# Optimization experiments

Hardware: AMD Instinct MI355X
Metric: run time of the kernel (lower is better)

The kernel has to match this reference:

```python
import jax, jax.numpy as jnp
import numpy as np

TOP_K = 2


def setup_inputs() -> dict:
    key = jax.random.key(0)
    ks = jax.random.split(key, 5)
    B, S, H, E, F = 2, 4096, 2048, 8, 4096
    scale_h = 1.0 / np.sqrt(H)
    scale_f = 1.0 / np.sqrt(F)
    return {
        "hidden_states": jax.random.normal(ks[0], (B, S, H), jnp.float32),
        "gate_w": jax.random.normal(ks[1], (E, H), jnp.float32) * scale_h,
        "w1": jax.random.normal(ks[2], (E, F, H), jnp.float32) * scale_h,
        "w3": jax.random.normal(ks[3], (E, F, H), jnp.float32) * scale_h,
        "w2": jax.random.normal(ks[4], (E, H, F), jnp.float32) * scale_f,
    }


def reference(hidden_states, gate_w, w1, w3, w2):
    B, S, H = hidden_states.shape
    E = gate_w.shape[0]
    x = hidden_states.reshape(-1, H)                      # [T, H]
    T = x.shape[0]

    # Router: logits -> softmax(fp32) -> top-k -> renormalize
    router_logits = x @ gate_w.T                          # [T, E]
    probs = jax.nn.softmax(router_logits.astype(jnp.float32), axis=-1)
    topk_w, topk_idx = jax.lax.top_k(probs, TOP_K)        # [T, k]
    topk_w = topk_w / jnp.sum(topk_w, axis=-1, keepdims=True)
    topk_w = topk_w.astype(x.dtype)

    # Per-expert combine weight (0 for unselected experts) [T, E]
    combine = jnp.sum(jax.nn.one_hot(topk_idx, E, dtype=x.dtype)
                      * topk_w[..., None], axis=1)

    # Expert SwiGLU MLPs, weighted-accumulated (loop over fixed E=8)
    out = jnp.zeros((T, H), dtype=x.dtype)
    for e in range(E):
        h = jax.nn.silu(x @ w1[e].T) * (x @ w3[e].T)      # [T, F]
        out = out + (h @ w2[e].T) * combine[:, e:e + 1]   # [T, H]

    return out.reshape(B, S, H), router_logits
```

## Files before the change

### kernel.cpp

```cpp
#include <hip/hip_runtime.h>
#include <math.h>

#define T_TOK 8192
#define H_DIM 2048
#define F_DIM 4096
#define E_NUM 8
#define MAXPAIR (T_TOK * 2)
#define MAX_MT 136
#define BM 128
#define BN 128
#define BK 32

typedef __attribute__((ext_vector_type(4))) float f32x4;
typedef __attribute__((ext_vector_type(8))) short s16x8;
typedef __attribute__((ext_vector_type(8))) __bf16 bf16x8;
typedef __attribute__((ext_vector_type(4))) unsigned short u16x4;

__device__ __forceinline__ unsigned short f2bf(float f) {
  unsigned int u = __float_as_uint(f);
  u += 0x7FFFu + ((u >> 16) & 1u);
  return (unsigned short)(u >> 16);
}

__device__ __forceinline__ s16x8 pack8(f32x4 a, f32x4 b) {
  s16x8 r;
  r[0] = (short)f2bf(a.x); r[1] = (short)f2bf(a.y);
  r[2] = (short)f2bf(a.z); r[3] = (short)f2bf(a.w);
  r[4] = (short)f2bf(b.x); r[5] = (short)f2bf(b.y);
  r[6] = (short)f2bf(b.z); r[7] = (short)f2bf(b.w);
  return r;
}

#define GLD16(gsrc, ldst)                                                      \
  __builtin_amdgcn_global_load_lds(                                            \
      (__attribute__((address_space(1))) void*)(gsrc),                         \
      (__attribute__((address_space(3))) void*)(ldst), 16, 0, 0)

__global__ __launch_bounds__(256) void convert_kernel(
    const float* __restrict__ src, unsigned short* __restrict__ dst,
    long long n8) {
  long long i = (long long)blockIdx.x * 256 + threadIdx.x;
  const long long stride = (long long)gridDim.x * 256;
  for (; i < n8; i += stride) {
    f32x4 a = *(const f32x4*)(src + i * 8);
    f32x4 b = *(const f32x4*)(src + i * 8 + 4);
    *(s16x8*)(dst + i * 8) = pack8(a, b);
  }
}

__global__ __launch_bounds__(256) void router_kernel(
    const float* __restrict__ x, const float* __restrict__ gw,
    float* __restrict__ logits, unsigned short* __restrict__ xb,
    int* __restrict__ ctrl, int* __restrict__ tIdx, float* __restrict__ tW) {
  const int wid = threadIdx.x >> 6, lane = threadIdx.x & 63;
  const int t = blockIdx.x * 4 + wid;
  const float* xr = x + (size_t)t * H_DIM;
  float acc[E_NUM];
#pragma unroll
  for (int e = 0; e < E_NUM; ++e) acc[e] = 0.f;
#pragma unroll
  for (int c = 0; c < H_DIM / 256; ++c) {
    const int h0 = c * 256 + lane * 4;
    f32x4 xv = *(const f32x4*)(xr + h0);
    u16x4 p;
    p.x = f2bf(xv.x); p.y = f2bf(xv.y); p.z = f2bf(xv.z); p.w = f2bf(xv.w);
    *(u16x4*)(xb + (size_t)t * H_DIM + h0) = p;
#pragma unroll
    for (int e = 0; e < E_NUM; ++e) {
      f32x4 gv = *(const f32x4*)(gw + (size_t)e * H_DIM + h0);
      acc[e] += xv.x * gv.x + xv.y * gv.y + xv.z * gv.z + xv.w * gv.w;
    }
  }
#pragma unroll
  for (int e = 0; e < E_NUM; ++e) {
#pragma unroll
    for (int off = 32; off >= 1; off >>= 1) acc[e] += __shfl_xor(acc[e], off, 64);
  }
  if (lane == 0) {
#pragma unroll
    for (int e = 0; e < E_NUM; ++e) logits[(size_t)t * E_NUM + e] = acc[e];
    int i0 = 0;
    float m0 = acc[0];
    for (int e = 1; e < E_NUM; ++e)
      if (acc[e] > m0) { m0 = acc[e]; i0 = e; }
    int i1 = -1;
    float m1 = -3.4e38f;
    for (int e = 0; e < E_NUM; ++e)
      if (e != i0 && acc[e] > m1) { m1 = acc[e]; i1 = e; }
    float ex = expf(m1 - m0);
    float w0 = 1.f / (1.f + ex);
    float w1 = ex * w0;
    tIdx[t * 2] = i0; tIdx[t * 2 + 1] = i1;
    tW[t * 2] = w0;  tW[t * 2 + 1] = w1;
    atomicAdd(&ctrl[i0], 1);
    atomicAdd(&ctrl[i1], 1);
  }
}

__global__ __launch_bounds__(256) void plan_kernel(int* __restrict__ ctrl) {
  __shared__ int cnt[E_NUM], offs[E_NUM + 1], tbase[E_NUM + 1];
  const int t = threadIdx.x;
  if (t < E_NUM) cnt[t] = ctrl[t];
  __syncthreads();
  if (t == 0) {
    int off = 0, mt = 0;
    for (int e = 0; e < E_NUM; ++e) {
      offs[e] = off; tbase[e] = mt;
      ctrl[8 + e] = off;
      ctrl[16 + e] = off;
      off += cnt[e];
      mt += (cnt[e] + BM - 1) / BM;
    }
    offs[E_NUM] = off; tbase[E_NUM] = mt;
    ctrl[24] = mt;
  }
  __syncthreads();
  const int total = tbase[E_NUM];
  for (int i = t; i < total; i += 256) {
    int e = 0;
    while (tbase[e + 1] <= i) ++e;
    ctrl[32 + i] = e;
    ctrl[32 + MAX_MT + i] = offs[e] + (i - tbase[e]) * BM;
  }
}

__global__ __launch_bounds__(256) void scatter_kernel(
    const int* __restrict__ tIdx, const float* __restrict__ tW,
    int* __restrict__ ctrl, int* __restrict__ pairTok,
    float* __restrict__ pairWgt) {
  const int t = blockIdx.x * 256 + threadIdx.x;
  if (t >= T_TOK) return;
#pragma unroll
  for (int j = 0; j < 2; ++j) {
    const int e = tIdx[t * 2 + j];
    const int pos = atomicAdd(&ctrl[16 + e], 1);
    pairTok[pos] = t;
    pairWgt[pos] = tW[t * 2 + j];
  }
}

template <int BBF>
__global__ __launch_bounds__(256, 2) void gemm1_kernel(
    const float* __restrict__ w1f, const float* __restrict__ w3f,
    const unsigned short* __restrict__ w1b,
    const unsigned short* __restrict__ w3b,
    const unsigned short* __restrict__ xb, const int* __restrict__ ctrl,
    const int* __restrict__ pairTok, unsigned short* __restrict__ hbuf) {
  const int mtTotal = ctrl[24];
  const int mt = blockIdx.x >> 5;
  const int nt = blockIdx.x & 31;
  if (mt >= mtTotal) return;
  const int e = ctrl[32 + mt];
  const int mbase = ctrl[32 + MAX_MT + mt];
  int mValid = ctrl[8 + e] + ctrl[e] - mbase;
  if (mValid > BM) mValid = BM;
  const int nbase = nt * BN;

  __shared__ __align__(16) short sA[3][BM * BK];
  __shared__ __align__(16) short sB1[3][BM * BK];
  __shared__ __align__(16) short sB3[3][BM * BK];
  __shared__ int sTok[BM];

  const int tid = threadIdx.x;
  if (tid < BM) sTok[tid] = pairTok[mbase + (tid < mValid ? tid : 0)];
  __syncthreads();

  const int c0 = tid, c1 = tid + 256;
  const int r0 = c0 >> 2, r1 = c1 >> 2;
  const int kg0 = (c0 & 3) ^ ((r0 >> 1) & 3);
  const int kg1 = (c1 & 3) ^ ((r1 >> 1) & 3);

  const unsigned short* srcA0 = xb + (size_t)sTok[r0] * H_DIM + kg0 * 8;
  const unsigned short* srcA1 = xb + (size_t)sTok[r1] * H_DIM + kg1 * 8;
  const size_t wbase = (size_t)e * F_DIM * H_DIM;
  const float *f10, *f11, *f30, *f31;
  const unsigned short *p10, *p11, *p30, *p31;
  if constexpr (BBF) {
    p10 = w1b + wbase + (size_t)(nbase + r0) * H_DIM + kg0 * 8;
    p11 = w1b + wbase + (size_t)(nbase + r1) * H_DIM + kg1 * 8;
    p30 = w3b + wbase + (size_t)(nbase + r0) * H_DIM + kg0 * 8;
    p31 = w3b + wbase + (size_t)(nbase + r1) * H_DIM + kg1 * 8;
  } else {
    f10 = w1f + wbase + (size_t)(nbase + r0) * H_DIM + kg0 * 8;
    f11 = w1f + wbase + (size_t)(nbase + r1) * H_DIM + kg1 * 8;
    f30 = w3f + wbase + (size_t)(nbase + r0) * H_DIM + kg0 * 8;
    f31 = w3f + wbase + (size_t)(nbase + r1) * H_DIM + kg1 * 8;
  }

  f32x4 acc1[4][4], acc3[4][4];
  const f32x4 fz = {0.f, 0.f, 0.f, 0.f};
#pragma unroll
  for (int i = 0; i < 4; ++i)
#pragma unroll
    for (int j = 0; j < 4; ++j) { acc1[i][j] = fz; acc3[i][j] = fz; }

  const int lane = tid & 63, wid = tid >> 6;
  const int wm = (wid >> 1) * 64, wn = (wid & 1) * 64;
  const int rl = lane & 15, kq = lane >> 4;

  int aIdx[4], bIdx[4];
#pragma unroll
  for (int i = 0; i < 4; ++i) {
    const int ra = wm + i * 16 + rl;
    aIdx[i] = ra * BK + ((kq ^ ((ra >> 1) & 3)) * 8);
    const int rb = wn + i * 16 + rl;
    bIdx[i] = rb * BK + ((kq ^ ((rb >> 1) & 3)) * 8);
  }

#define STAGE1(buf, k0)                                                        \
  {                                                                            \
    GLD16(srcA0 + (k0), &sA[buf][c0 * 8]);                                     \
    GLD16(srcA1 + (k0), &sA[buf][c1 * 8]);                                     \
    if constexpr (BBF) {                                                       \
      GLD16(p10 + (k0), &sB1[buf][c0 * 8]);                                    \
      GLD16(p11 + (k0), &sB1[buf][c1 * 8]);                                    \
      GLD16(p30 + (k0), &sB3[buf][c0 * 8]);                                    \
      GLD16(p31 + (k0), &sB3[buf][c1 * 8]);                                    \
    } else {                                                                   \
      f32x4 t0 = *(const f32x4*)(f10 + (k0));                                  \
      f32x4 t1 = *(const f32x4*)(f10 + (k0) + 4);                              \
      *(s16x8*)&sB1[buf][c0 * 8] = pack8(t0, t1);                              \
      t0 = *(const f32x4*)(f11 + (k0));                                        \
      t1 = *(const f32x4*)(f11 + (k0) + 4);                                    \
      *(s16x8*)&sB1[buf][c1 * 8] = pack8(t0, t1);                              \
      t0 = *(const f32x4*)(f30 + (k0));                                        \
      t1 = *(const f32x4*)(f30 + (k0) + 4);                                    \
      *(s16x8*)&sB3[buf][c0 * 8] = pack8(t0, t1);                              \
      t0 = *(const f32x4*)(f31 + (k0));                                        \
      t1 = *(const f32x4*)(f31 + (k0) + 4);                                    \
      *(s16x8*)&sB3[buf][c1 * 8] = pack8(t0, t1);                              \
    }                                                                          \
  }

  STAGE1(0, 0);
  STAGE1(1, BK);

  const int NS = H_DIM / BK;
  int cur = 0;
  for (int s = 0; s < NS; ++s) {
    if (s + 2 < NS) {
      const int nxt = (cur + 2 >= 3) ? cur - 1 : cur + 2;
      STAGE1(nxt, (s + 2) * BK);
      if constexpr (BBF)
        asm volatile("s_waitcnt vmcnt(12)" ::: "memory");
      else
        asm volatile("s_waitcnt vmcnt(0) lgkmcnt(0)" ::: "memory");
    } else if (s + 2 == NS) {
      if constexpr (BBF)
        asm volatile("s_waitcnt vmcnt(6)" ::: "memory");
      else
        asm volatile("s_waitcnt vmcnt(0) lgkmcnt(0)" ::: "memory");
    } else {
      asm volatile("s_waitcnt vmcnt(0) lgkmcnt(0)" ::: "memory");
    }
    __builtin_amdgcn_s_barrier();
    asm volatile("" ::: "memory");

    bf16x8 af[4], bf1[4], bf3[4];
#pragma unroll
    for (int i = 0; i < 4; ++i) {
      af[i] = *(const bf16x8*)&sA[cur][aIdx[i]];
      bf1[i] = *(const bf16x8*)&sB1[cur][bIdx[i]];
      bf3[i] = *(const bf16x8*)&sB3[cur][bIdx[i]];
    }
    __builtin_amdgcn_s_setprio(1);
#pragma unroll
    for (int mr = 0; mr < 4; ++mr)
#pragma unroll
      for (int nr = 0; nr < 4; ++nr) {
        acc1[mr][nr] = __builtin_amdgcn_mfma_f32_16x16x32_bf16(
            af[mr], bf1[nr], acc1[mr][nr], 0, 0, 0);
        acc3[mr][nr] = __builtin_amdgcn_mfma_f32_16x16x32_bf16(
            af[mr], bf3[nr], acc3[mr][nr], 0, 0, 0);
      }
    __builtin_amdgcn_s_setprio(0);
    asm volatile("" ::: "memory");
    __builtin_amdgcn_s_barrier();
    cur = (cur + 1 >= 3) ? 0 : cur + 1;
  }

#pragma unroll
  for (int mr = 0; mr < 4; ++mr) {
#pragma unroll
    for (int j = 0; j < 4; ++j) {
      const int row = wm + mr * 16 + kq * 4 + j;
      if (row < mValid) {
        unsigned short* dst =
            hbuf + (size_t)(mbase + row) * F_DIM + nbase + wn + rl;
#pragma unroll
        for (int nr = 0; nr < 4; ++nr) {
          const float z = acc1[mr][nr][j];
          const float hv = (z / (1.f + expf(-z))) * acc3[mr][nr][j];
          dst[nr * 16] = f2bf(hv);
        }
      }
    }
  }
#undef STAGE1
}

template <int BBF>
__global__ __launch_bounds__(256, 2) void gemm2_kernel(
    const float* __restrict__ w2f, const unsigned short* __restrict__ w2b,
    const unsigned short* __restrict__ hbuf, const int* __restrict__ ctrl,
    const int* __restrict__ pairTok, const float* __restrict__ pairWgt,
    float* __restrict__ out) {
  const int mtTotal = ctrl[24];
  const int mt = blockIdx.x >> 4;
  const int nt = blockIdx.x & 15;
  if (mt >= mtTotal) return;
  const int e = ctrl[32 + mt];
  const int mbase = ctrl[32 + MAX_MT + mt];
  int mValid = ctrl[8 + e] + ctrl[e] - mbase;
  if (mValid > BM) mValid = BM;
  const int nbase = nt * BN;

  __shared__ __align__(16) short sA[3][BM * BK];
  __shared__ __align__(16) short sB[3][BM * BK];
  __shared__ int sTok[BM];
  __shared__ float sWgt[BM];

  const int tid = threadIdx.x;
  if (tid < BM) {
    const int p = mbase + (tid < mValid ? tid : 0);
    sTok[tid] = pairTok[p];
    sWgt[tid] = pairWgt[p];
  }
  __syncthreads();

  const int c0 = tid, c1 = tid + 256;
  const int r0 = c0 >> 2, r1 = c1 >> 2;
  const int kg0 = (c0 & 3) ^ ((r0 >> 1) & 3);
  const int kg1 = (c1 & 3) ^ ((r1 >> 1) & 3);

  size_t pa0 = (size_t)(mbase + r0); if (pa0 > MAXPAIR - 1) pa0 = MAXPAIR - 1;
  size_t pa1 = (size_t)(mbase + r1); if (pa1 > MAXPAIR - 1) pa1 = MAXPAIR - 1;
  const unsigned short* srcA0 = hbuf + pa0 * F_DIM + kg0 * 8;
  const unsigned short* srcA1 = hbuf + pa1 * F_DIM + kg1 * 8;
  const size_t wbase = (size_t)e * H_DIM * F_DIM;
  const float *fw0, *fw1;
  const unsigned short *pw0, *pw1;
  if constexpr (BBF) {
    pw0 = w2b + wbase + (size_t)(nbase + r0) * F_DIM + kg0 * 8;
    pw1 = w2b + wbase + (size_t)(nbase + r1) * F_DIM + kg1 * 8;
  } else {
    fw0 = w2f + wbase + (size_t)(nbase + r0) * F_DIM + kg0 * 8;
    fw1 = w2f + wbase + (size_t)(nbase + r1) * F_DIM + kg1 * 8;
  }

  f32x4 acc[4][4];
  const f32x4 fz = {0.f, 0.f, 0.f, 0.f};
#pragma unroll
  for (int i = 0; i < 4; ++i)
#pragma unroll
    for (int j = 0; j < 4; ++j) acc[i][j] = fz;

  const int lane = tid & 63, wid = tid >> 6;
  const int wm = (wid >> 1) * 64, wn = (wid & 1) * 64;
  const int rl = lane & 15, kq = lane >> 4;

  int aIdx[4], bIdx[4];
#pragma unroll
  for (int i = 0; i < 4; ++i) {
    const int ra = wm + i * 16 + rl;
    aIdx[i] = ra * BK + ((kq ^ ((ra >> 1) & 3)) * 8);
    const int rb = wn + i * 16 + rl;
    bIdx[i] = rb * BK + ((kq ^ ((rb >> 1) & 3)) * 8);
  }

#define STAGE2(buf, k0)                                                        \
  {                                                                            \
    GLD16(srcA0 + (k0), &sA[buf][c0 * 8]);                                     \
    GLD16(srcA1 + (k0), &sA[buf][c1 * 8]);                                     \
    if constexpr (BBF) {                                                       \
      GLD16(pw0 + (k0), &sB[buf][c0 * 8]);                                     \
      GLD16(pw1 + (k0), &sB[buf][c1 * 8]);                                     \
    } else {                                                                   \
      f32x4 t0 = *(const f32x4*)(fw0 + (k0));                                  \
      f32x4 t1 = *(const f32x4*)(fw0 + (k0) + 4);                              \
      *(s16x8*)&sB[buf][c0 * 8] = pack8(t0, t1);                               \
      t0 = *(const f32x4*)(fw1 + (k0));                                        \
      t1 = *(const f32x4*)(fw1 + (k0) + 4);                                    \
      *(s16x8*)&sB[buf][c1 * 8] = pack8(t0, t1);                               \
    }                                                                          \
  }

  STAGE2(0, 0);
  STAGE2(1, BK);

  const int NS = F_DIM / BK;
  int cur = 0;
  for (int s = 0; s < NS; ++s) {
    if (s + 2 < NS) {
      const int nxt = (cur + 2 >= 3) ? cur - 1 : cur + 2;
      STAGE2(nxt, (s + 2) * BK);
      if constexpr (BBF)
        asm volatile("s_waitcnt vmcnt(8)" ::: "memory");
      else
        asm volatile("s_waitcnt vmcnt(0) lgkmcnt(0)" ::: "memory");
    } else if (s + 2 == NS) {
      if constexpr (BBF)
        asm volatile("s_waitcnt vmcnt(4)" ::: "memory");
      else
        asm volatile("s_waitcnt vmcnt(0) lgkmcnt(0)" ::: "memory");
    } else {
      asm volatile("s_waitcnt vmcnt(0) lgkmcnt(0)" ::: "memory");
    }
    __builtin_amdgcn_s_barrier();
    asm volatile("" ::: "memory");

    bf16x8 af[4], bf[4];
#pragma unroll
    for (int i = 0; i < 4; ++i) {
      af[i] = *(const bf16x8*)&sA[cur][aIdx[i]];
      bf[i] = *(const bf16x8*)&sB[cur][bIdx[i]];
    }
    __builtin_amdgcn_s_setprio(1);
#pragma unroll
    for (int mr = 0; mr < 4; ++mr)
#pragma unroll
      for (int nr = 0; nr < 4; ++nr)
        acc[mr][nr] = __builtin_amdgcn_mfma_f32_16x16x32_bf16(
            af[mr], bf[nr], acc[mr][nr], 0, 0, 0);
    __builtin_amdgcn_s_setprio(0);
    asm volatile("" ::: "memory");
    __builtin_amdgcn_s_barrier();
    cur = (cur + 1 >= 3) ? 0 : cur + 1;
  }

#pragma unroll
  for (int mr = 0; mr < 4; ++mr) {
#pragma unroll
    for (int j = 0; j < 4; ++j) {
      const int row = wm + mr * 16 + kq * 4 + j;
      if (row < mValid) {
        const int tok = sTok[row];
        const float w = sWgt[row];
        float* dst = out + (size_t)tok * H_DIM + nbase + wn + rl;
#pragma unroll
        for (int nr = 0; nr < 4; ++nr)
          unsafeAtomicAdd(dst + nr * 16, w * acc[mr][nr][j]);
      }
    }
  }
#undef STAGE2
}

extern "C" void kernel_launch(void* const* d_in, const int* in_sizes, int n_in,
                              void* d_out, int out_size, void* d_ws,
                              size_t ws_size, hipStream_t stream) {
  const float* x  = (const float*)d_in[0];
  const float* gw = (const float*)d_in[1];
  const float* w1 = (const float*)d_in[2];
  const float* w3 = (const float*)d_in[3];
  const float* w2 = (const float*)d_in[4];
  float* out = (float*)d_out;
  float* logits = out + (size_t)T_TOK * H_DIM;

  char* ws = (char*)d_ws;
  const size_t HDR = 1u << 20;
  const size_t XB_SZ = (size_t)T_TOK * H_DIM * 2;
  const size_t HB_SZ = (size_t)MAXPAIR * F_DIM * 2;
  const size_t W_SZ  = (size_t)E_NUM * F_DIM * H_DIM * 2;

  int* ctrl = (int*)(ws);
  int* tIdx = (int*)(ws + 4096);
  float* tW = (float*)(ws + 4096 + 65536);
  int* pairTok = (int*)(ws + 4096 + 131072);
  float* pairWgt = (float*)(ws + 4096 + 196608);
  unsigned short* xb = (unsigned short*)(ws + HDR);
  unsigned short* hbuf = (unsigned short*)(ws + HDR + XB_SZ);
  unsigned short* w1b = (unsigned short*)(ws + HDR + XB_SZ + HB_SZ);
  unsigned short* w3b = w1b + W_SZ / 2;
  unsigned short* w2b = w3b + W_SZ / 2;

  const bool cw13 = ws_size >= HDR + XB_SZ + HB_SZ + 2 * W_SZ;
  const bool cw2  = ws_size >= HDR + XB_SZ + HB_SZ + 3 * W_SZ;

  hipMemsetAsync(ctrl, 0, 4096, stream);
  hipMemsetAsync(out, 0, (size_t)T_TOK * H_DIM * sizeof(float), stream);

  const long long N8 = (long long)E_NUM * F_DIM * H_DIM / 8;
  if (cw13) {
    convert_kernel<<<2048, 256, 0, stream>>>(w1, w1b, N8);
    convert_kernel<<<2048, 256, 0, stream>>>(w3, w3b, N8);
  }
  if (cw2) convert_kernel<<<2048, 256, 0, stream>>>(w2, w2b, N8);

  router_kernel<<<T_TOK / 4, 256, 0, stream>>>(x, gw, logits, xb, ctrl, tIdx, tW);
  plan_kernel<<<1, 256, 0, stream>>>(ctrl);
  scatter_kernel<<<T_TOK / 256, 256, 0, stream>>>(tIdx, tW, ctrl, pairTok, pairWgt);

  if (cw13)
    gemm1_kernel<1><<<MAX_MT * 32, 256, 0, stream>>>(w1, w3, w1b, w3b, xb, ctrl,
                                                     pairTok, hbuf);
  else
    gemm1_kernel<0><<<MAX_MT * 32, 256, 0, stream>>>(w1, w3, w1b, w3b, xb, ctrl,
                                                     pairTok, hbuf);
  if (cw2)
    gemm2_kernel<1><<<MAX_MT * 16, 256, 0, stream>>>(w2, w2b, hbuf, ctrl,
                                                     pairTok, pairWgt, out);
  else
    gemm2_kernel<0><<<MAX_MT * 16, 256, 0, stream>>>(w2, w2b, hbuf, ctrl,
                                                     pairTok, pairWgt, out);
}
```

Measured before the change: 1.580 ms.

## Fold w2 bf16 conversion into gemm1 grid to overlap with compute

Removes the standalone w2 fp32-to-bf16 conversion launch and runs that work on extra blocks inside the gemm1 launch. Every third block among the first 3*NCONV does conversion and the rest map onto the gemm1 tiles. The memory-bound conversion can then overlap the compute-bound grouped GEMM instead of running serially. The cost is more complex block indexing and conversion blocks competing with gemm1 blocks for CUs and bandwidth.

```diff
diff --git a/kernel.cpp b/kernel.cpp
--- a/kernel.cpp
+++ b/kernel.cpp
@@ -10,6 +10,7 @@
 #define BM 128
 #define BN 128
 #define BK 32
+#define NCONV 2048
 
 typedef __attribute__((ext_vector_type(4))) float f32x4;
 typedef __attribute__((ext_vector_type(8))) short s16x8;
@@ -145,10 +146,32 @@
     const unsigned short* __restrict__ w1b,
     const unsigned short* __restrict__ w3b,
     const unsigned short* __restrict__ xb, const int* __restrict__ ctrl,
-    const int* __restrict__ pairTok, unsigned short* __restrict__ hbuf) {
+    const int* __restrict__ pairTok, unsigned short* __restrict__ hbuf,
+    const float* __restrict__ w2f, unsigned short* __restrict__ w2b,
+    int nconv) {
+  int gid = blockIdx.x;
+  const int nconv3 = nconv * 3;
+  if (gid < nconv3) {
+    if ((gid % 3) == 2) {
+      const int cid = gid / 3;
+      const long long per = (long long)E_NUM * F_DIM * H_DIM / 8 / NCONV;
+      long long i = (long long)cid * per + threadIdx.x;
+      const long long end = (long long)(cid + 1) * per;
+      for (; i < end; i += 256) {
+        f32x4 a = *(const f32x4*)(w2f + i * 8);
+        f32x4 b = *(const f32x4*)(w2f + i * 8 + 4);
+        *(s16x8*)(w2b + i * 8) = pack8(a, b);
+      }
+      return;
+    }
+    gid = gid - (gid + 1) / 3;
+  } else {
+    gid = gid - nconv;
+  }
+
   const int mtTotal = ctrl[24];
-  const int mt = blockIdx.x >> 5;
-  const int nt = blockIdx.x & 31;
+  const int mt = gid >> 5;
+  const int nt = gid & 31;
   if (mt >= mtTotal) return;
   const int e = ctrl[32 + mt];
   const int mbase = ctrl[32 + MAX_MT + mt];
@@ -485,18 +508,20 @@
     convert_kernel<<<2048, 256, 0, stream>>>(w1, w1b, N8);
     convert_kernel<<<2048, 256, 0, stream>>>(w3, w3b, N8);
   }
-  if (cw2) convert_kernel<<<2048, 256, 0, stream>>>(w2, w2b, N8);
 
   router_kernel<<<T_TOK / 4, 256, 0, stream>>>(x, gw, logits, xb, ctrl, tIdx, tW);
   plan_kernel<<<1, 256, 0, stream>>>(ctrl);
   scatter_kernel<<<T_TOK / 256, 256, 0, stream>>>(tIdx, tW, ctrl, pairTok, pairWgt);
 
-  if (cw13)
-    gemm1_kernel<1><<<MAX_MT * 32, 256, 0, stream>>>(w1, w3, w1b, w3b, xb, ctrl,
-                                                     pairTok, hbuf);
-  else
-    gemm1_kernel<0><<<MAX_MT * 32, 256, 0, stream>>>(w1, w3, w1b, w3b, xb, ctrl,
-                                                     pairTok, hbuf);
+  const int NG = MAX_MT * 32;
+  if (cw13) {
+    const int nconv = cw2 ? NCONV : 0;
+    gemm1_kernel<1><<<NG + nconv, 256, 0, stream>>>(
+        w1, w3, w1b, w3b, xb, ctrl, pairTok, hbuf, w2, w2b, nconv);
+  } else {
+    gemm1_kernel<0><<<NG, 256, 0, stream>>>(
+        w1, w3, w1b, w3b, xb, ctrl, pairTok, hbuf, w2, w2b, 0);
+  }
   if (cw2)
     gemm2_kernel<1><<<MAX_MT * 16, 256, 0, stream>>>(w2, w2b, hbuf, ctrl,
                                                      pairTok, pairWgt, out);
```

Result: faster. 1.548 ms (-2.0%).
